# Optimization experiments

Hardware: AMD Instinct MI355X
Metric: run time of the kernel (lower is better)

## Reference

```python
import jax, jax.numpy as jnp
import numpy as np

B, S, HID = 1, 2048, 2048
H, KVH, HD = 32, 8, 64
THETA = 10000.0


def _rotate_half(x):
    x1, x2 = jnp.split(x, 2, axis=-1)
    return jnp.concatenate([-x2, x1], axis=-1)


def _rope_cos_sin(seq_len, head_dim, theta, dtype):
    inv_freq = 1.0 / (theta ** (jnp.arange(0, head_dim, 2, dtype=jnp.float32) / head_dim))
    pos = jnp.arange(seq_len, dtype=jnp.float32)
    freqs = pos[:, None] * inv_freq[None, :]          # [S, HD/2]
    emb = jnp.concatenate([freqs, freqs], axis=-1)     # [S, HD]
    return jnp.cos(emb).astype(dtype), jnp.sin(emb).astype(dtype)


def setup_inputs() -> dict:
    key = jax.random.key(0)
    k0, k1, k2, k3, k4 = jax.random.split(key, 5)
    w = lambda k, shape: jax.random.normal(k, shape, dtype=jnp.float32) * 0.02
    return {
        "hidden_states": jax.random.normal(k0, (B, S, HID), dtype=jnp.float32),
        "Wq": w(k1, (H * HD, HID)),
        "Wk": w(k2, (KVH * HD, HID)),
        "Wv": w(k3, (KVH * HD, HID)),
        "Wo": w(k4, (HID, H * HD)),
    }


def reference(hidden_states, Wq, Wk, Wv, Wo):
    b, s, _ = hidden_states.shape
    dtype = hidden_states.dtype

    # QKV projections (nn.Linear, bias=False -> x @ W.T)
    q = (hidden_states @ Wq.T).reshape(b, s, H, HD).transpose(0, 2, 1, 3)    # [b,H,s,d]
    k = (hidden_states @ Wk.T).reshape(b, s, KVH, HD).transpose(0, 2, 1, 3)  # [b,KVH,s,d]
    v = (hidden_states @ Wv.T).reshape(b, s, KVH, HD).transpose(0, 2, 1, 3)

    # RoPE (prefill: position_ids = arange(s))
    cos, sin = _rope_cos_sin(s, HD, THETA, dtype)  # [s, HD]
    apply_rope = lambda x: x * cos + _rotate_half(x) * sin
    q = apply_rope(q)
    k = apply_rope(k)

    # GQA: repeat KV heads to match query heads
    groups = H // KVH
    k = jnp.repeat(k, groups, axis=1)  # [b,H,s,d]
    v = jnp.repeat(v, groups, axis=1)

    scale = 1.0 / jnp.sqrt(jnp.asarray(HD, dtype=dtype))
    logits = jnp.einsum('bhqd,bhkd->bhqk', q, k) * scale  # [b,H,s,s]

    # prefill causal mask (phys_past_len = 0)
    causal = jnp.tril(jnp.ones((s, s), dtype=bool))
    logits = jnp.where(causal, logits, jnp.finfo(dtype).min)

    attn = jax.nn.softmax(logits, axis=-1)
    out = jnp.einsum('bhqk,bhkd->bhqd', attn, v)            # [b,H,s,d]
    out = out.transpose(0, 2, 1, 3).reshape(b, s, H * HD)   # [b,s,hidden]
    return out @ Wo.T
```

## Files before the change

### kernel.cpp

```cpp
#include <hip/hip_runtime.h>
#include <hip/hip_bf16.h>
#include <cstdint>
#include <cstddef>

#define SEQ   2048
#define HID   2048
#define NH    32
#define NKVH  8
#define HD    64
#define KVDIM (NKVH * HD)

typedef __bf16 bf16_t;
typedef __bf16 bf16x8 __attribute__((ext_vector_type(8)));
typedef float  f32x4  __attribute__((ext_vector_type(4)));

#define ROPE_L 0.4152410118609203f

#if __has_builtin(__builtin_amdgcn_exp2f)
#define QSCALE 0.18033688011112043f
#define EXPFN(x) __builtin_amdgcn_exp2f(x)
#else
#define QSCALE 0.125f
#define EXPFN(x) __expf(x)
#endif

__device__ __forceinline__ bf16x8 load8(const float* p) {
    const float4 lo = *(const float4*)p;
    const float4 hi = *(const float4*)(p + 4);
    bf16x8 r;
    r[0] = (bf16_t)lo.x; r[1] = (bf16_t)lo.y; r[2] = (bf16_t)lo.z; r[3] = (bf16_t)lo.w;
    r[4] = (bf16_t)hi.x; r[5] = (bf16_t)hi.y; r[6] = (bf16_t)hi.z; r[7] = (bf16_t)hi.w;
    return r;
}

__device__ __forceinline__ void load_lds16(const bf16_t* g, bf16_t* l) {
    __builtin_amdgcn_global_load_lds((const __attribute__((address_space(1))) void*)g,
                                     (__attribute__((address_space(3))) void*)l,
                                     16, 0, 0);
}

#define NX  (SEQ * HID)
#define NWQ (NH * HD * HID)
#define NWK (KVDIM * HID)
#define NWV (KVDIM * HID)
#define NWO (HID * NH * HD)
#define NTOT (NX + NWQ + NWK + NWV + NWO)

__global__ __launch_bounds__(256) void cvt_all(const float* __restrict__ X,
                                               const float* __restrict__ Wq,
                                               const float* __restrict__ Wk,
                                               const float* __restrict__ Wv,
                                               const float* __restrict__ Wo,
                                               bf16_t* __restrict__ Xb,
                                               bf16_t* __restrict__ Wqb,
                                               bf16_t* __restrict__ Wkb,
                                               bf16_t* __restrict__ Wvb,
                                               bf16_t* __restrict__ Wob)
{
    size_t i = ((size_t)blockIdx.x * 256 + threadIdx.x) * 8;
    if (i >= NTOT) return;
    const size_t E0 = NX, E1 = E0 + NWQ, E2 = E1 + NWK, E3 = E2 + NWV;
    const float* s; bf16_t* d; size_t off;
    if (i < E0)      { s = X;  d = Xb;  off = i; }
    else if (i < E1) { s = Wq; d = Wqb; off = i - E0; }
    else if (i < E2) { s = Wk; d = Wkb; off = i - E1; }
    else if (i < E3) { s = Wv; d = Wvb; off = i - E2; }
    else             { s = Wo; d = Wob; off = i - E3; }
    *(bf16x8*)(d + off) = load8(s + off);
}


__global__ __launch_bounds__(256) void qkv_gemm(const bf16_t* __restrict__ Xb,
                                                const bf16_t* __restrict__ Wqb,
                                                const bf16_t* __restrict__ Wkb,
                                                const bf16_t* __restrict__ Wvb,
                                                bf16_t* __restrict__ Qb,
                                                bf16_t* __restrict__ Kb,
                                                bf16_t* __restrict__ Vt)
{
    __shared__ alignas(16) bf16_t sa0[128 * 64], sa1[128 * 64];
    __shared__ alignas(16) bf16_t sb0[64 * 64],  sb1[64 * 64];
    const int t = threadIdx.x;
    const int lane = t & 63;
    const int w  = t >> 6;
    const int n16 = lane & 15;
    const int q4  = lane >> 4;
    f32x4 acc[2][4] = {};

    const int m0 = blockIdx.x * 128;
    const int n0 = blockIdx.y * 64;

    const bf16_t* B;
    int mode, nc;
    if (n0 < NH * HD)              { B = Wqb + (size_t)n0 * HID;                     mode = 0; nc = n0; }
    else if (n0 < NH * HD + KVDIM) { B = Wkb + (size_t)(n0 - NH * HD) * HID;         mode = 1; nc = n0 - NH * HD; }
    else                           { B = Wvb + (size_t)(n0 - NH * HD - KVDIM) * HID; mode = 2; nc = n0 - NH * HD - KVDIM; }

    const int lrow8 = lane >> 3;
    const int lgrp  = (lane & 7) ^ lrow8;
    const bf16_t* ag = Xb + (size_t)(m0 + w * 8 + lrow8) * HID + lgrp * 8;
    const bf16_t* bg = B  + (size_t)(w * 8 + lrow8) * HID + lgrp * 8;

    auto stage = [&](bf16_t* da, bf16_t* db, int k0) {
#pragma unroll
        for (int s = 0; s < 4; ++s)
            load_lds16(ag + (size_t)(s * 32) * HID + k0, da + (w * 8 + s * 32) * 64);
#pragma unroll
        for (int s = 0; s < 2; ++s)
            load_lds16(bg + (size_t)(s * 32) * HID + k0, db + (w * 8 + s * 32) * 64);
    };
    auto mma_step = [&](const bf16_t* sa, const bf16_t* sb) {
#pragma unroll
        for (int kk = 0; kk < 2; ++kk) {
            const int xo = ((kk * 4 + q4) ^ (n16 & 7)) * 8;
            bf16x8 bfrag[4];
#pragma unroll
            for (int j = 0; j < 4; ++j)
                bfrag[j] = *(const bf16x8*)&sb[(j * 16 + n16) * 64 + xo];
#pragma unroll
            for (int i = 0; i < 2; ++i) {
                bf16x8 af = *(const bf16x8*)&sa[(w * 32 + i * 16 + n16) * 64 + xo];
#pragma unroll
                for (int j = 0; j < 4; ++j)
                    acc[i][j] = __builtin_amdgcn_mfma_f32_16x16x32_bf16(af, bfrag[j], acc[i][j], 0, 0, 0);
            }
        }
    };

    stage(sa0, sb0, 0);
    __syncthreads();
    for (int k0 = 0; k0 < HID; k0 += 128) {
        if (k0 + 64 < HID) stage(sa1, sb1, k0 + 64);
        mma_step(sa0, sb0);
        __syncthreads();
        if (k0 + 128 < HID) stage(sa0, sb0, k0 + 128);
        mma_step(sa1, sb1);
        __syncthreads();
    }

    if (mode < 2) {
#pragma unroll
        for (int jt = 0; jt < 2; ++jt) {
            float dd = (float)(jt * 16 + n16);
            float inv = exp2f(-dd * ROPE_L);
#pragma unroll
            for (int i = 0; i < 2; ++i) {
#pragma unroll
                for (int r = 0; r < 4; ++r) {
                    int pos = m0 + w * 32 + i * 16 + q4 * 4 + r;
                    float ang = (float)pos * inv;
                    float sn, cs;
                    sincosf(ang, &sn, &cs);
                    float x1 = acc[i][jt][r], x2 = acc[i][jt + 2][r];
                    acc[i][jt][r]     = x1 * cs - x2 * sn;
                    acc[i][jt + 2][r] = x2 * cs + x1 * sn;
                }
            }
        }
        const float osc = (mode == 0) ? QSCALE : 1.0f;
        bf16_t* dst = (mode == 0) ? Qb : Kb;
        const int ld = (mode == 0) ? NH * HD : KVDIM;
#pragma unroll
        for (int i = 0; i < 2; ++i)
#pragma unroll
            for (int j = 0; j < 4; ++j) {
                int row = m0 + w * 32 + i * 16 + q4 * 4;
                int col = nc + j * 16 + n16;
#pragma unroll
                for (int r = 0; r < 4; ++r)
                    dst[(size_t)(row + r) * ld + col] = (bf16_t)(acc[i][j][r] * osc);
            }
    } else {
#pragma unroll
        for (int i = 0; i < 2; ++i)
#pragma unroll
            for (int j = 0; j < 4; ++j) {
                int row = m0 + w * 32 + i * 16 + q4 * 4;
                int col = nc + j * 16 + n16;
#pragma unroll
                for (int r = 0; r < 4; ++r)
                    Vt[(size_t)col * SEQ + row + r] = (bf16_t)acc[i][j][r];
            }
    }
}

__global__ __launch_bounds__(256) void o_gemm(const bf16_t* __restrict__ A,
                                              const bf16_t* __restrict__ Bw,
                                              float* __restrict__ C)
{
    __shared__ alignas(16) bf16_t sa0[128 * 64], sa1[128 * 64];
    __shared__ alignas(16) bf16_t sb0[64 * 64],  sb1[64 * 64];
    const int t = threadIdx.x;
    const int lane = t & 63;
    const int w  = t >> 6;
    const int n16 = lane & 15;
    const int q4  = lane >> 4;
    f32x4 acc[2][4] = {};

    const int m0 = blockIdx.x * 128;
    const int n0 = blockIdx.y * 64;

    const int lrow8 = lane >> 3;
    const int lgrp  = (lane & 7) ^ lrow8;
    const bf16_t* ag = A  + (size_t)(m0 + w * 8 + lrow8) * HID + lgrp * 8;
    const bf16_t* bg = Bw + (size_t)(n0 + w * 8 + lrow8) * HID + lgrp * 8;

    auto stage = [&](bf16_t* da, bf16_t* db, int k0) {
#pragma unroll
        for (int s = 0; s < 4; ++s)
            load_lds16(ag + (size_t)(s * 32) * HID + k0, da + (w * 8 + s * 32) * 64);
#pragma unroll
        for (int s = 0; s < 2; ++s)
            load_lds16(bg + (size_t)(s * 32) * HID + k0, db + (w * 8 + s * 32) * 64);
    };
    auto mma_step = [&](const bf16_t* sa, const bf16_t* sb) {
#pragma unroll
        for (int kk = 0; kk < 2; ++kk) {
            const int xo = ((kk * 4 + q4) ^ (n16 & 7)) * 8;
            bf16x8 bfrag[4];
#pragma unroll
            for (int j = 0; j < 4; ++j)
                bfrag[j] = *(const bf16x8*)&sb[(j * 16 + n16) * 64 + xo];
#pragma unroll
            for (int i = 0; i < 2; ++i) {
                bf16x8 af = *(const bf16x8*)&sa[(w * 32 + i * 16 + n16) * 64 + xo];
#pragma unroll
                for (int j = 0; j < 4; ++j)
                    acc[i][j] = __builtin_amdgcn_mfma_f32_16x16x32_bf16(af, bfrag[j], acc[i][j], 0, 0, 0);
            }
        }
    };

    stage(sa0, sb0, 0);
    __syncthreads();
    for (int k0 = 0; k0 < HID; k0 += 128) {
        if (k0 + 64 < HID) stage(sa1, sb1, k0 + 64);
        mma_step(sa0, sb0);
        __syncthreads();
        if (k0 + 128 < HID) stage(sa0, sb0, k0 + 128);
        mma_step(sa1, sb1);
        __syncthreads();
    }

#pragma unroll
    for (int i = 0; i < 2; ++i)
#pragma unroll
        for (int j = 0; j < 4; ++j) {
            int row = m0 + w * 32 + i * 16 + q4 * 4;
            int col = n0 + j * 16 + n16;
#pragma unroll
            for (int r = 0; r < 4; ++r)
                C[(size_t)(row + r) * HID + col] = acc[i][j][r];
        }
}

__global__ __launch_bounds__(256, 3) void attn_mfma(const bf16_t* __restrict__ Qm,
                                                    const bf16_t* __restrict__ Km,
                                                    const bf16_t* __restrict__ Vt,
                                                    bf16_t* __restrict__ Om)
{
    const int bid = blockIdx.x;
    const int h   = bid & (NH - 1);
    const int qt  = (bid < (SEQ / 128) * NH / 2)
                      ? (SEQ / 128 - 1 - (bid >> 5))
                      : ((bid - (SEQ / 128) * NH / 2) >> 5);
    const int q0  = qt * 128;
    const int kvh = h >> 2;
    const int t    = threadIdx.x;
    const int w    = t >> 6;
    const int lane = t & 63;
    const int n16  = lane & 15;
    const int q4   = lane >> 4;

    __shared__ alignas(16) bf16_t kb0[64 * 64], kb1[64 * 64];
    __shared__ alignas(16) bf16_t vb0[64 * 64], vb1[64 * 64];
    __shared__ alignas(16) bf16_t ps[4][2][32 * 40];

    bf16x8 qf[2][2];
#pragma unroll
    for (int i = 0; i < 2; ++i) {
        const bf16_t* qp = Qm + (size_t)(q0 + w * 32 + i * 16 + n16) * HID + h * HD;
        qf[i][0] = *(const bf16x8*)(qp + q4 * 8);
        qf[i][1] = *(const bf16x8*)(qp + 32 + q4 * 8);
    }

    f32x4 acc[2][4] = {};
    f32x4 acc_l[2] = {};
    const bf16_t one = (bf16_t)1.0f;
    const bf16x8 ones8 = {one, one, one, one, one, one, one, one};

    const int lrow8 = lane >> 3;
    const int lgrp  = (lane & 7) ^ lrow8;
    const bf16_t* kgs = Km + (size_t)kvh * HD + (size_t)lrow8 * KVDIM + lgrp * 8;
    const bf16_t* vgs = Vt + (size_t)(kvh * HD + lrow8) * SEQ + lgrp * 8;

    const int rx  = n16 & 7;
    const int xo0 = (q4 ^ rx) * 8;
    const int xo1 = ((q4 + 4) ^ rx) * 8;

    const int ghmax  = 2 * qt + 1;
    const int my_last = 2 * qt + (w >> 1);
    const int wkey   = (q4 & 2) << 3;
    const int rdkey  = ((n16 >> 2) & 2) << 3;

    auto stage = [&](int gh, bf16_t* kb, bf16_t* vb) {
        const int k0 = gh * 64;
        load_lds16(kgs + (size_t)(k0 + w * 8)      * KVDIM, kb + (w * 8)      * 64);
        load_lds16(kgs + (size_t)(k0 + w * 8 + 32) * KVDIM, kb + (w * 8 + 32) * 64);
        load_lds16(vgs + (size_t)(w * 8)      * SEQ + k0,   vb + (w * 8)      * 64);
        load_lds16(vgs + (size_t)(w * 8 + 32) * SEQ + k0,   vb + (w * 8 + 32) * 64);
    };

    auto compute = [&](int gh, const bf16_t* kbuf, const bf16_t* vbuf) {
        f32x4 st[2][4];
        __builtin_amdgcn_s_setprio(1);
#pragma unroll
        for (int jt = 0; jt < 4; ++jt) {
            bf16x8 kf0 = *(const bf16x8*)&kbuf[(jt * 16 + n16) * 64 + xo0];
            bf16x8 kf1 = *(const bf16x8*)&kbuf[(jt * 16 + n16) * 64 + xo1];
#pragma unroll
            for (int i = 0; i < 2; ++i) {
                f32x4 s = {};
                s = __builtin_amdgcn_mfma_f32_16x16x32_bf16(qf[i][0], kf0, s, 0, 0, 0);
                s = __builtin_amdgcn_mfma_f32_16x16x32_bf16(qf[i][1], kf1, s, 0, 0, 0);
                st[i][jt] = s;
            }
        }
        __builtin_amdgcn_s_setprio(0);

        if (gh == my_last) {
#pragma unroll
            for (int i = 0; i < 2; ++i) {
                int rowb = q0 + w * 32 + i * 16 + q4 * 4;
#pragma unroll
                for (int jt = 0; jt < 4; ++jt) {
                    int colg = gh * 64 + jt * 16 + n16;
#pragma unroll
                    for (int r = 0; r < 4; ++r)
                        if (colg > rowb + r) st[i][jt][r] = -1e30f;
                }
            }
        }

#pragma unroll
        for (int i = 0; i < 2; ++i)
#pragma unroll
            for (int jt = 0; jt < 4; ++jt)
#pragma unroll
                for (int r = 0; r < 4; ++r)
                    st[i][jt][r] = EXPFN(st[i][jt][r]);

#pragma unroll
        for (int i = 0; i < 2; ++i)
#pragma unroll
            for (int jt = 0; jt < 4; ++jt) {
                bf16_t* ph = ps[w][jt >> 1];
                int rowb = i * 16 + q4 * 4;
                int csw  = ((jt & 1) * 16 + n16) ^ wkey;
#pragma unroll
                for (int r = 0; r < 4; ++r)
                    ph[(rowb + r) * 40 + csw] = (bf16_t)st[i][jt][r];
            }

        bf16x8 pf[2][2];
#pragma unroll
        for (int i = 0; i < 2; ++i) {
            int ra = (i * 16 + n16) * 40 + ((q4 * 8) ^ rdkey);
            pf[i][0] = *(const bf16x8*)&ps[w][0][ra];
            pf[i][1] = *(const bf16x8*)&ps[w][1][ra];
        }

        __builtin_amdgcn_s_setprio(1);
#pragma unroll
        for (int i = 0; i < 2; ++i) {
            acc_l[i] = __builtin_amdgcn_mfma_f32_16x16x32_bf16(pf[i][0], ones8, acc_l[i], 0, 0, 0);
            acc_l[i] = __builtin_amdgcn_mfma_f32_16x16x32_bf16(pf[i][1], ones8, acc_l[i], 0, 0, 0);
        }
#pragma unroll
        for (int jd = 0; jd < 4; ++jd) {
            bf16x8 vf0 = *(const bf16x8*)&vbuf[(jd * 16 + n16) * 64 + xo0];
            bf16x8 vf1 = *(const bf16x8*)&vbuf[(jd * 16 + n16) * 64 + xo1];
#pragma unroll
            for (int i = 0; i < 2; ++i) {
                acc[i][jd] = __builtin_amdgcn_mfma_f32_16x16x32_bf16(pf[i][0], vf0, acc[i][jd], 0, 0, 0);
                acc[i][jd] = __builtin_amdgcn_mfma_f32_16x16x32_bf16(pf[i][1], vf1, acc[i][jd], 0, 0, 0);
            }
        }
        __builtin_amdgcn_s_setprio(0);
    };

    stage(0, kb0, vb0);
    __syncthreads();
    for (int gh = 0; gh <= ghmax; gh += 2) {
        if (gh < ghmax) stage(gh + 1, kb1, vb1);
        if (gh <= my_last) compute(gh, kb0, vb0);
        __syncthreads();
        if (gh + 1 < ghmax) stage(gh + 2, kb0, vb0);
        if (gh + 1 <= my_last) compute(gh + 1, kb1, vb1);
        __syncthreads();
    }

#pragma unroll
    for (int i = 0; i < 2; ++i) {
        float linv[4];
#pragma unroll
        for (int r = 0; r < 4; ++r) linv[r] = 1.0f / acc_l[i][r];
#pragma unroll
        for (int jd = 0; jd < 4; ++jd)
#pragma unroll
            for (int r = 0; r < 4; ++r) {
                int rowg = q0 + w * 32 + i * 16 + q4 * 4 + r;
                Om[(size_t)rowg * HID + h * HD + jd * 16 + n16] = (bf16_t)(acc[i][jd][r] * linv[r]);
            }
    }
}

extern "C" void kernel_launch(void* const* d_in, const int* in_sizes, int n_in,
                              void* d_out, int out_size, void* d_ws, size_t ws_size,
                              hipStream_t stream)
{
    const float* X  = (const float*)d_in[0];
    const float* Wq = (const float*)d_in[1];
    const float* Wk = (const float*)d_in[2];
    const float* Wv = (const float*)d_in[3];
    const float* Wo = (const float*)d_in[4];
    float* out = (float*)d_out;

    bf16_t* Xb  = (bf16_t*)d_ws;
    bf16_t* Wqb = Xb  + (size_t)NX;
    bf16_t* Wkb = Wqb + (size_t)NWQ;
    bf16_t* Wvb = Wkb + (size_t)NWK;
    bf16_t* Wob = Wvb + (size_t)NWV;
    bf16_t* Qb  = Wob + (size_t)NWO;
    bf16_t* Kb  = Qb  + (size_t)SEQ * (NH * HD);
    bf16_t* Vt  = Kb  + (size_t)SEQ * KVDIM;
    bf16_t* Ob  = Vt  + (size_t)SEQ * KVDIM;

    dim3 blk(256);

    cvt_all<<<dim3((NTOT / 8 + 255) / 256), blk, 0, stream>>>(X, Wq, Wk, Wv, Wo, Xb, Wqb, Wkb, Wvb, Wob);

    qkv_gemm<<<dim3(SEQ / 128, (NH * HD + 2 * KVDIM) / 64), blk, 0, stream>>>(Xb, Wqb, Wkb, Wvb, Qb, Kb, Vt);

    attn_mfma<<<dim3((SEQ / 128) * NH), blk, 0, stream>>>(Qb, Kb, Vt, Ob);

    o_gemm<<<dim3(SEQ / 128, HID / 64), blk, 0, stream>>>(Ob, Wob, out);
}
```

Before: 196.5 us.

## Enlarge GEMM tiles to 128x128 and transpose score MFMA for packed P stores

The QKV and output projection GEMMs now use 128x128 block tiles, with each wave computing a 64x64 sub-tile from 4x4 MFMA fragments. This raises arithmetic intensity per LDS load and halves the grid size. In attention, the QK^T MFMA operands are swapped so each lane holds four consecutive key positions. The probabilities can then be packed with v_cvt_pk_bf16_f32 and written as 8-byte stores into a padded LDS buffer instead of scalar swizzled stores. The risks are higher register pressure, fewer blocks for occupancy and tail effects, and changed LDS bank-conflict behaviour.

New measurement: 194.2 us. Within noise of the previous version (-1.2%).

```diff
diff --git a/kernel.cpp b/kernel.cpp
--- a/kernel.cpp
+++ b/kernel.cpp
@@ -13,6 +13,7 @@
 typedef __bf16 bf16_t;
 typedef __bf16 bf16x8 __attribute__((ext_vector_type(8)));
 typedef float  f32x4  __attribute__((ext_vector_type(4)));
+typedef unsigned int u32x2 __attribute__((ext_vector_type(2)));
 
 #define ROPE_L 0.4152410118609203f
 
@@ -37,6 +38,12 @@
     __builtin_amdgcn_global_load_lds((const __attribute__((address_space(1))) void*)g,
                                      (__attribute__((address_space(3))) void*)l,
                                      16, 0, 0);
+}
+
+__device__ __forceinline__ unsigned int cvt_pk_bf16(float lo, float hi) {
+    unsigned int r;
+    asm("v_cvt_pk_bf16_f32 %0, %1, %2" : "=v"(r) : "v"(lo), "v"(hi));
+    return r;
 }
 
 #define NX  (SEQ * HID)
@@ -70,25 +77,27 @@
 }
 
 
-__global__ __launch_bounds__(256) void qkv_gemm(const bf16_t* __restrict__ Xb,
-                                                const bf16_t* __restrict__ Wqb,
-                                                const bf16_t* __restrict__ Wkb,
-                                                const bf16_t* __restrict__ Wvb,
-                                                bf16_t* __restrict__ Qb,
-                                                bf16_t* __restrict__ Kb,
-                                                bf16_t* __restrict__ Vt)
+__global__ __launch_bounds__(256, 2) void qkv_gemm(const bf16_t* __restrict__ Xb,
+                                                   const bf16_t* __restrict__ Wqb,
+                                                   const bf16_t* __restrict__ Wkb,
+                                                   const bf16_t* __restrict__ Wvb,
+                                                   bf16_t* __restrict__ Qb,
+                                                   bf16_t* __restrict__ Kb,
+                                                   bf16_t* __restrict__ Vt)
 {
     __shared__ alignas(16) bf16_t sa0[128 * 64], sa1[128 * 64];
-    __shared__ alignas(16) bf16_t sb0[64 * 64],  sb1[64 * 64];
+    __shared__ alignas(16) bf16_t sb0[128 * 64], sb1[128 * 64];
     const int t = threadIdx.x;
     const int lane = t & 63;
     const int w  = t >> 6;
     const int n16 = lane & 15;
     const int q4  = lane >> 4;
-    f32x4 acc[2][4] = {};
+    const int wm = (w >> 1) * 64;
+    const int wn = (w & 1) * 64;
+    f32x4 acc[4][4] = {};
 
     const int m0 = blockIdx.x * 128;
-    const int n0 = blockIdx.y * 64;
+    const int n0 = blockIdx.y * 128;
 
     const bf16_t* B;
     int mode, nc;
@@ -103,27 +112,27 @@
 
     auto stage = [&](bf16_t* da, bf16_t* db, int k0) {
 #pragma unroll
-        for (int s = 0; s < 4; ++s)
+        for (int s = 0; s < 4; ++s) {
             load_lds16(ag + (size_t)(s * 32) * HID + k0, da + (w * 8 + s * 32) * 64);
-#pragma unroll
-        for (int s = 0; s < 2; ++s)
             load_lds16(bg + (size_t)(s * 32) * HID + k0, db + (w * 8 + s * 32) * 64);
+        }
     };
     auto mma_step = [&](const bf16_t* sa, const bf16_t* sb) {
 #pragma unroll
         for (int kk = 0; kk < 2; ++kk) {
             const int xo = ((kk * 4 + q4) ^ (n16 & 7)) * 8;
-            bf16x8 bfrag[4];
+            bf16x8 bfrag[4], afrag[4];
 #pragma unroll
             for (int j = 0; j < 4; ++j)
-                bfrag[j] = *(const bf16x8*)&sb[(j * 16 + n16) * 64 + xo];
-#pragma unroll
-            for (int i = 0; i < 2; ++i) {
-                bf16x8 af = *(const bf16x8*)&sa[(w * 32 + i * 16 + n16) * 64 + xo];
+                bfrag[j] = *(const bf16x8*)&sb[(wn + j * 16 + n16) * 64 + xo];
+#pragma unroll
+            for (int i = 0; i < 4; ++i)
+                afrag[i] = *(const bf16x8*)&sa[(wm + i * 16 + n16) * 64 + xo];
+#pragma unroll
+            for (int i = 0; i < 4; ++i)
 #pragma unroll
                 for (int j = 0; j < 4; ++j)
-                    acc[i][j] = __builtin_amdgcn_mfma_f32_16x16x32_bf16(af, bfrag[j], acc[i][j], 0, 0, 0);
-            }
+                    acc[i][j] = __builtin_amdgcn_mfma_f32_16x16x32_bf16(afrag[i], bfrag[j], acc[i][j], 0, 0, 0);
         }
     };
 
@@ -144,10 +153,10 @@
             float dd = (float)(jt * 16 + n16);
             float inv = exp2f(-dd * ROPE_L);
 #pragma unroll
-            for (int i = 0; i < 2; ++i) {
+            for (int i = 0; i < 4; ++i) {
 #pragma unroll
                 for (int r = 0; r < 4; ++r) {
-                    int pos = m0 + w * 32 + i * 16 + q4 * 4 + r;
+                    int pos = m0 + wm + i * 16 + q4 * 4 + r;
                     float ang = (float)pos * inv;
                     float sn, cs;
                     sincosf(ang, &sn, &cs);
@@ -161,22 +170,22 @@
         bf16_t* dst = (mode == 0) ? Qb : Kb;
         const int ld = (mode == 0) ? NH * HD : KVDIM;
 #pragma unroll
-        for (int i = 0; i < 2; ++i)
+        for (int i = 0; i < 4; ++i)
 #pragma unroll
             for (int j = 0; j < 4; ++j) {
-                int row = m0 + w * 32 + i * 16 + q4 * 4;
-                int col = nc + j * 16 + n16;
+                int row = m0 + wm + i * 16 + q4 * 4;
+                int col = nc + wn + j * 16 + n16;
 #pragma unroll
                 for (int r = 0; r < 4; ++r)
                     dst[(size_t)(row + r) * ld + col] = (bf16_t)(acc[i][j][r] * osc);
             }
     } else {
 #pragma unroll
-        for (int i = 0; i < 2; ++i)
+        for (int i = 0; i < 4; ++i)
 #pragma unroll
             for (int j = 0; j < 4; ++j) {
-                int row = m0 + w * 32 + i * 16 + q4 * 4;
-                int col = nc + j * 16 + n16;
+                int row = m0 + wm + i * 16 + q4 * 4;
+                int col = nc + wn + j * 16 + n16;
 #pragma unroll
                 for (int r = 0; r < 4; ++r)
                     Vt[(size_t)col * SEQ + row + r] = (bf16_t)acc[i][j][r];
@@ -184,21 +193,23 @@
     }
 }
 
-__global__ __launch_bounds__(256) void o_gemm(const bf16_t* __restrict__ A,
-                                              const bf16_t* __restrict__ Bw,
-                                              float* __restrict__ C)
+__global__ __launch_bounds__(256, 2) void o_gemm(const bf16_t* __restrict__ A,
+                                                 const bf16_t* __restrict__ Bw,
+                                                 float* __restrict__ C)
 {
     __shared__ alignas(16) bf16_t sa0[128 * 64], sa1[128 * 64];
-    __shared__ alignas(16) bf16_t sb0[64 * 64],  sb1[64 * 64];
+    __shared__ alignas(16) bf16_t sb0[128 * 64], sb1[128 * 64];
     const int t = threadIdx.x;
     const int lane = t & 63;
     const int w  = t >> 6;
     const int n16 = lane & 15;
     const int q4  = lane >> 4;
-    f32x4 acc[2][4] = {};
+    const int wm = (w >> 1) * 64;
+    const int wn = (w & 1) * 64;
+    f32x4 acc[4][4] = {};
 
     const int m0 = blockIdx.x * 128;
-    const int n0 = blockIdx.y * 64;
+    const int n0 = blockIdx.y * 128;
 
     const int lrow8 = lane >> 3;
     const int lgrp  = (lane & 7) ^ lrow8;
@@ -207,27 +218,27 @@
 
     auto stage = [&](bf16_t* da, bf16_t* db, int k0) {
 #pragma unroll
-        for (int s = 0; s < 4; ++s)
+        for (int s = 0; s < 4; ++s) {
             load_lds16(ag + (size_t)(s * 32) * HID + k0, da + (w * 8 + s * 32) * 64);
-#pragma unroll
-        for (int s = 0; s < 2; ++s)
             load_lds16(bg + (size_t)(s * 32) * HID + k0, db + (w * 8 + s * 32) * 64);
+        }
     };
     auto mma_step = [&](const bf16_t* sa, const bf16_t* sb) {
 #pragma unroll
         for (int kk = 0; kk < 2; ++kk) {
             const int xo = ((kk * 4 + q4) ^ (n16 & 7)) * 8;
-            bf16x8 bfrag[4];
+            bf16x8 bfrag[4], afrag[4];
 #pragma unroll
             for (int j = 0; j < 4; ++j)
-                bfrag[j] = *(const bf16x8*)&sb[(j * 16 + n16) * 64 + xo];
-#pragma unroll
-            for (int i = 0; i < 2; ++i) {
-                bf16x8 af = *(const bf16x8*)&sa[(w * 32 + i * 16 + n16) * 64 + xo];
+                bfrag[j] = *(const bf16x8*)&sb[(wn + j * 16 + n16) * 64 + xo];
+#pragma unroll
+            for (int i = 0; i < 4; ++i)
+                afrag[i] = *(const bf16x8*)&sa[(wm + i * 16 + n16) * 64 + xo];
+#pragma unroll
+            for (int i = 0; i < 4; ++i)
 #pragma unroll
                 for (int j = 0; j < 4; ++j)
-                    acc[i][j] = __builtin_amdgcn_mfma_f32_16x16x32_bf16(af, bfrag[j], acc[i][j], 0, 0, 0);
-            }
+                    acc[i][j] = __builtin_amdgcn_mfma_f32_16x16x32_bf16(afrag[i], bfrag[j], acc[i][j], 0, 0, 0);
         }
     };
 
@@ -243,16 +254,18 @@
     }
 
 #pragma unroll
-    for (int i = 0; i < 2; ++i)
+    for (int i = 0; i < 4; ++i)
 #pragma unroll
         for (int j = 0; j < 4; ++j) {
-            int row = m0 + w * 32 + i * 16 + q4 * 4;
-            int col = n0 + j * 16 + n16;
+            int row = m0 + wm + i * 16 + q4 * 4;
+            int col = n0 + wn + j * 16 + n16;
 #pragma unroll
             for (int r = 0; r < 4; ++r)
                 C[(size_t)(row + r) * HID + col] = acc[i][j][r];
         }
 }
+
+#define PLD 72
 
 __global__ __launch_bounds__(256, 3) void attn_mfma(const bf16_t* __restrict__ Qm,
                                                     const bf16_t* __restrict__ Km,
@@ -274,7 +287,7 @@
 
     __shared__ alignas(16) bf16_t kb0[64 * 64], kb1[64 * 64];
     __shared__ alignas(16) bf16_t vb0[64 * 64], vb1[64 * 64];
-    __shared__ alignas(16) bf16_t ps[4][2][32 * 40];
+    __shared__ alignas(16) bf16_t ps[4][32 * PLD];
 
     bf16x8 qf[2][2];
 #pragma unroll
@@ -300,8 +313,6 @@
 
     const int ghmax  = 2 * qt + 1;
     const int my_last = 2 * qt + (w >> 1);
-    const int wkey   = (q4 & 2) << 3;
-    const int rdkey  = ((n16 >> 2) & 2) << 3;
 
     auto stage = [&](int gh, bf16_t* kb, bf16_t* vb) {
         const int k0 = gh * 64;
@@ -321,8 +332,8 @@
 #pragma unroll
             for (int i = 0; i < 2; ++i) {
                 f32x4 s = {};
-                s = __builtin_amdgcn_mfma_f32_16x16x32_bf16(qf[i][0], kf0, s, 0, 0, 0);
-                s = __builtin_amdgcn_mfma_f32_16x16x32_bf16(qf[i][1], kf1, s, 0, 0, 0);
+                s = __builtin_amdgcn_mfma_f32_16x16x32_bf16(kf0, qf[i][0], s, 0, 0, 0);
+                s = __builtin_amdgcn_mfma_f32_16x16x32_bf16(kf1, qf[i][1], s, 0, 0, 0);
                 st[i][jt] = s;
             }
         }
@@ -331,13 +342,13 @@
         if (gh == my_last) {
 #pragma unroll
             for (int i = 0; i < 2; ++i) {
-                int rowb = q0 + w * 32 + i * 16 + q4 * 4;
+                int qg = q0 + w * 32 + i * 16 + n16;
 #pragma unroll
                 for (int jt = 0; jt < 4; ++jt) {
-                    int colg = gh * 64 + jt * 16 + n16;
+                    int kvb = gh * 64 + jt * 16 + q4 * 4;
 #pragma unroll
                     for (int r = 0; r < 4; ++r)
-                        if (colg > rowb + r) st[i][jt][r] = -1e30f;
+                        if (kvb + r > qg) st[i][jt][r] = -1e30f;
                 }
             }
         }
@@ -351,23 +362,23 @@
                     st[i][jt][r] = EXPFN(st[i][jt][r]);
 
 #pragma unroll
-        for (int i = 0; i < 2; ++i)
+        for (int i = 0; i < 2; ++i) {
+            bf16_t* pr = &ps[w][(i * 16 + n16) * PLD];
 #pragma unroll
             for (int jt = 0; jt < 4; ++jt) {
-                bf16_t* ph = ps[w][jt >> 1];
-                int rowb = i * 16 + q4 * 4;
-                int csw  = ((jt & 1) * 16 + n16) ^ wkey;
-#pragma unroll
-                for (int r = 0; r < 4; ++r)
-                    ph[(rowb + r) * 40 + csw] = (bf16_t)st[i][jt][r];
-            }
+                u32x2 pw;
+                pw[0] = cvt_pk_bf16(st[i][jt][0], st[i][jt][1]);
+                pw[1] = cvt_pk_bf16(st[i][jt][2], st[i][jt][3]);
+                *(u32x2*)&pr[jt * 16 + q4 * 4] = pw;
+            }
+        }
 
         bf16x8 pf[2][2];
 #pragma unroll
         for (int i = 0; i < 2; ++i) {
-            int ra = (i * 16 + n16) * 40 + ((q4 * 8) ^ rdkey);
-            pf[i][0] = *(const bf16x8*)&ps[w][0][ra];
-            pf[i][1] = *(const bf16x8*)&ps[w][1][ra];
+            const bf16_t* pr = &ps[w][(i * 16 + n16) * PLD];
+            pf[i][0] = *(const bf16x8*)&pr[q4 * 8];
+            pf[i][1] = *(const bf16x8*)&pr[32 + q4 * 8];
         }
 
         __builtin_amdgcn_s_setprio(1);
@@ -440,9 +451,9 @@
 
     cvt_all<<<dim3((NTOT / 8 + 255) / 256), blk, 0, stream>>>(X, Wq, Wk, Wv, Wo, Xb, Wqb, Wkb, Wvb, Wob);
 
-    qkv_gemm<<<dim3(SEQ / 128, (NH * HD + 2 * KVDIM) / 64), blk, 0, stream>>>(Xb, Wqb, Wkb, Wvb, Qb, Kb, Vt);
+    qkv_gemm<<<dim3(SEQ / 128, (NH * HD + 2 * KVDIM) / 128), blk, 0, stream>>>(Xb, Wqb, Wkb, Wvb, Qb, Kb, Vt);
 
     attn_mfma<<<dim3((SEQ / 128) * NH), blk, 0, stream>>>(Qb, Kb, Vt, Ob);
 
-    o_gemm<<<dim3(SEQ / 128, HID / 64), blk, 0, stream>>>(Ob, Wob, out);
-}
+    o_gemm<<<dim3(SEQ / 128, HID / 128), blk, 0, stream>>>(Ob, Wob, out);
+}
```
